# Performance work log

Measured on AMD Instinct MI355X. Metric: run time of the kernel, lower is better.

The kernel has to match this reference:

```python
import jax, jax.numpy as jnp
from jax import lax
import numpy as np

B, N, FIN, T, K, C_CHEB, F_TIME, STRIDE = 32, 900, 16, 24, 3, 64, 64, 1
LN_EPS = 1e-5


def _cheb_polys(L_tilde, K):
    # Faithful to repo: recurrence uses ELEMENTWISE multiply (np.ndarray '*').
    polys = [np.identity(N), np.asarray(L_tilde)]
    for i in range(2, K):
        polys.append(2 * L_tilde * polys[i - 1] - polys[i - 2])
    return np.stack(polys, axis=0).astype(np.float32)  # (K, N, N)


def setup_inputs() -> dict:
    key = jax.random.key(0)
    ks = jax.random.split(key, 6)
    rng = np.random.RandomState(0)
    A = rng.randn(N, N).astype(np.float32)
    L_tilde = (A + A.T) / (2.0 * np.sqrt(N))  # symmetric, entries O(1/sqrt(N))
    cheb = jnp.asarray(_cheb_polys(L_tilde, K))  # (K, N, N)
    x = jax.random.normal(ks[0], (B, N, FIN, T), dtype=jnp.float32)
    theta = jax.random.normal(ks[1], (K, FIN, C_CHEB), dtype=jnp.float32) * 0.1
    time_w = jax.random.normal(ks[2], (F_TIME, C_CHEB, 1, 3), dtype=jnp.float32) * 0.05
    time_b = jax.random.normal(ks[3], (F_TIME,), dtype=jnp.float32) * 0.01
    res_w = jax.random.normal(ks[4], (F_TIME, FIN, 1, 1), dtype=jnp.float32) * 0.1
    res_b = jax.random.normal(ks[5], (F_TIME,), dtype=jnp.float32) * 0.01
    gamma = jnp.ones((F_TIME,), dtype=jnp.float32)
    beta = jnp.zeros((F_TIME,), dtype=jnp.float32)
    return {"x": x, "cheb": cheb, "theta": theta, "time_w": time_w,
            "time_b": time_b, "res_w": res_w, "res_b": res_b,
            "gamma": gamma, "beta": beta}


def reference(x, cheb, theta, time_w, time_b, res_w, res_b, gamma, beta):
    b, n, f_in, t = x.shape
    # forward hardcodes spatial attention to ones
    spatial_at = jnp.ones((b, n, n), dtype=x.dtype)
    # Chebyshev graph conv with (trivial) spatial attention.
    # rhs[b,t,n,f] = sum_m (T_k * sA)[b,m,n] * x[b,m,f,t]
    out = jnp.zeros((b, t, n, theta.shape[-1]), dtype=x.dtype)
    for k in range(theta.shape[0]):
        Tk = cheb[k] * spatial_at                      # (B, N, N)
        rhs = jnp.einsum('bmn,bmft->btnf', Tk, x)      # (B, T, N, F_in)
        out = out + jnp.einsum('btnf,fc->btnc', rhs, theta[k])
    spatial_gcn = jax.nn.relu(out)                     # (B, T, N, C)
    # time conv over T axis: input layout (B, C, N, T), kernel (1,3), pad (0,1)
    g = jnp.transpose(spatial_gcn, (0, 3, 2, 1))       # (B, C, N, T)
    tc = lax.conv_general_dilated(g, time_w, window_strides=(1, STRIDE),
                                  padding=((0, 0), (1, 1)),
                                  dimension_numbers=('NCHW', 'OIHW', 'NCHW'))
    tc = tc + time_b[None, :, None, None]
    # residual 1x1 conv on raw input
    xr = jnp.transpose(x, (0, 2, 1, 3))                # (B, F_in, N, T)
    rc = lax.conv_general_dilated(xr, res_w, window_strides=(1, STRIDE),
                                  padding=((0, 0), (0, 0)),
                                  dimension_numbers=('NCHW', 'OIHW', 'NCHW'))
    rc = rc + res_b[None, :, None, None]
    y = jax.nn.relu(rc + tc)                           # (B, F_time, N, T)
    y = jnp.transpose(y, (0, 3, 2, 1))                 # (B, T, N, F_time)
    mu = jnp.mean(y, axis=-1, keepdims=True)
    var = jnp.mean(jnp.square(y - mu), axis=-1, keepdims=True)
    y_ln = (y - mu) * lax.rsqrt(var + LN_EPS) * gamma + beta
    return jnp.transpose(y_ln, (0, 2, 3, 1))           # (B, N, F_time, T)
```

## Files before the change

### kernel.cpp

```cpp
#include <hip/hip_runtime.h>
#include <hip/hip_bf16.h>

#define B_ 32
#define N_ 900
#define BN 8
#define NTILES 113
#define MS 16
#define MP 960

typedef __attribute__((ext_vector_type(8))) short bf16x8;
typedef __attribute__((ext_vector_type(16))) float f32x16;

#define OFF_XT 0u
#define OFF_CT 23592960u
#define OFF_XC 27279360u
#define OFF_TH 74465280u
#define OFF_TW 74472448u
#define WS_NEED 74500096u

__global__ __launch_bounds__(256)
void k0a_xT(const float* __restrict__ x, __hip_bfloat16* __restrict__ xT)
{
    __shared__ __hip_bfloat16 L[32][390];
    const int tid = threadIdx.x;
    const int m0 = blockIdx.x * 32, b = blockIdx.y;
#pragma unroll
    for (int it = 0; it < 12; ++it) {
        const int idx = tid + it * 256;
        const int mm = idx / 96, c4 = idx - mm * 96;
        float4 v = make_float4(0.f, 0.f, 0.f, 0.f);
        if (m0 + mm < N_)
            v = ((const float4*)(x + ((size_t)b * N_ + m0 + mm) * 384))[c4];
        L[mm][c4 * 4 + 0] = __float2bfloat16(v.x);
        L[mm][c4 * 4 + 1] = __float2bfloat16(v.y);
        L[mm][c4 * 4 + 2] = __float2bfloat16(v.z);
        L[mm][c4 * 4 + 3] = __float2bfloat16(v.w);
    }
    __syncthreads();
#pragma unroll
    for (int it = 0; it < 48; ++it) {
        const int idx = tid + it * 256;
        const int c = idx >> 5, mm = idx & 31;
        xT[((size_t)b * 384 + c) * MP + m0 + mm] = L[mm][c];
    }
}

__global__ __launch_bounds__(256)
void k0b_chebT(const float* __restrict__ cheb, __hip_bfloat16* __restrict__ chebT)
{
    __shared__ float L[32][33];
    const int tid = threadIdx.x;
    const int m0 = blockIdx.x * 32, n0 = blockIdx.y * 32, k = blockIdx.z;
#pragma unroll
    for (int it = 0; it < 4; ++it) {
        const int idx = tid + it * 256;
        const int mm = idx >> 5, nn = idx & 31;
        float v = 0.f;
        if (m0 + mm < N_ && n0 + nn < N_)
            v = cheb[(size_t)(k + 1) * (N_ * N_) + (size_t)(m0 + mm) * N_ + n0 + nn];
        L[mm][nn] = v;
    }
    __syncthreads();
#pragma unroll
    for (int it = 0; it < 4; ++it) {
        const int idx = tid + it * 256;
        const int nn = idx >> 5, mm = idx & 31;
        chebT[((size_t)k * MP + n0 + nn) * MP + m0 + mm] = __float2bfloat16(L[mm][nn]);
    }
}

__global__ __launch_bounds__(256)
void k0c_w(const float* __restrict__ tw, const float* __restrict__ rw,
           const float* __restrict__ th,
           __hip_bfloat16* __restrict__ thT, __hip_bfloat16* __restrict__ twB)
{
    const int tid = threadIdx.x;
    for (int i = tid; i < 64 * 56; i += 256) {
        const int c = i / 56, k = i - (i / 56) * 56;
        const float v = (k < 48) ? th[k * 64 + c] : 0.f;
        thT[i] = __float2bfloat16(v);
    }
    for (int i = tid; i < 64 * 216; i += 256) {
        const int co = i / 216, k = i - co * 216;
        float v = 0.f;
        if (k < 192)      v = tw[co * 192 + (k & 63) * 3 + (k >> 6)];
        else if (k < 208) v = rw[co * 16 + (k - 192)];
        twB[i] = __float2bfloat16(v);
    }
}

__global__ __launch_bounds__(512)
void k1_mfma(const __hip_bfloat16* __restrict__ xT,
             const __hip_bfloat16* __restrict__ chebT,
             __hip_bfloat16* __restrict__ xcb)
{
    __shared__ __align__(16) __hip_bfloat16 At[2][192][40];
    __shared__ __align__(16) __hip_bfloat16 Bt[2][128][40];
    const int tid = threadIdx.x;
    const int id  = blockIdx.x;
    const int swz  = (id & 7) * 120 + (id >> 3);
    const int tile = swz % 15;
    const int z    = swz / 15;
    const int n0 = (tile % 5) * 192;
    const int c0 = (tile / 5) * 128;
    const int b = z >> 1, k = z & 1;

    const int wid = tid >> 6, lane = tid & 63;
    const int wr = wid & 1, wc = wid >> 1;
    const int lr = lane & 31, hi = lane >> 5;

    const __hip_bfloat16* Asrc = chebT + ((size_t)k * MP + n0) * MP;
    const __hip_bfloat16* Bsrc = xT + ((size_t)b * 384 + c0) * MP;

    f32x16 acc[3];
#pragma unroll
    for (int rb = 0; rb < 3; ++rb)
#pragma unroll
        for (int j = 0; j < 16; ++j) acc[rb][j] = 0.f;

    auto stage = [&](int buf, int m0) {
        for (int q = tid; q < 768; q += 512) {
            const int r = q >> 2, c8 = (q & 3) * 8;
            *(int4*)&At[buf][r][c8] = *(const int4*)(Asrc + (size_t)r * MP + m0 + c8);
        }
        {
            const int q = tid;
            if (q < 512) {
                const int r = q >> 2, c8 = (q & 3) * 8;
                *(int4*)&Bt[buf][r][c8] = *(const int4*)(Bsrc + (size_t)r * MP + m0 + c8);
            }
        }
    };

    stage(0, 0);
    __syncthreads();
    for (int s = 0; s < 30; ++s) {
        if (s + 1 < 30) stage((s + 1) & 1, (s + 1) * 32);
        const int cur = s & 1;
#pragma unroll
        for (int ks = 0; ks < 2; ++ks) {
            const bf16x8 bb = *(const bf16x8*)&Bt[cur][wc * 32 + lr][ks * 16 + hi * 8];
#pragma unroll
            for (int rb = 0; rb < 3; ++rb) {
                const bf16x8 a =
                    *(const bf16x8*)&At[cur][wr * 96 + rb * 32 + lr][ks * 16 + hi * 8];
                acc[rb] = __builtin_amdgcn_mfma_f32_32x32x16_bf16(a, bb, acc[rb], 0, 0, 0);
            }
        }
        __syncthreads();
    }

    const int c = c0 + wc * 32 + lr;
    __hip_bfloat16* ob = xcb + ((size_t)(k * B_ + b)) * (MP * 384) + c;
#pragma unroll
    for (int rb = 0; rb < 3; ++rb)
#pragma unroll
        for (int reg = 0; reg < 16; ++reg) {
            const int row = n0 + wr * 96 + rb * 32 + (reg & 3) + 8 * (reg >> 2) + 4 * hi;
            ob[(size_t)row * 384] = __float2bfloat16(acc[rb][reg]);
        }
}

__global__ __launch_bounds__(384, 5)
void k2_mfma(const float* __restrict__ x,
             const __hip_bfloat16* __restrict__ xcb,
             const __hip_bfloat16* __restrict__ thT,
             const __hip_bfloat16* __restrict__ twB,
             const float* __restrict__ tb, const float* __restrict__ rb,
             const float* __restrict__ gam, const float* __restrict__ bet,
             float* __restrict__ out)
{
    __shared__ __align__(16) short xcL[2][8][384];
    __shared__ __align__(16) __hip_bfloat16 xbL[8][24][24];
    __shared__ __align__(16) __hip_bfloat16 gcnL[8][26][72];
    __shared__ float biasL[64], gamL[64], betL[64];

    const int tid = threadIdx.x;
    const int wid = tid >> 6, lane = tid & 63;
    const int l31 = lane & 31, hi = lane >> 5;
    const int n_base = blockIdx.x * BN;
    const int b = blockIdx.y;

    if (tid < 64) {
        biasL[tid] = tb[tid] + rb[tid];
        gamL[tid]  = gam[tid];
        betL[tid]  = bet[tid];
    }
    for (int q = tid; q < 768; q += 384) {
        const int kk = q / 384, r = q - kk * 384;
        const int nl = r / 48, ch = r - nl * 48;
        ((int4*)xcL)[q] =
            *(const int4*)(xcb + (((size_t)(kk * B_ + b)) * MP + n_base + nl) * 384 + ch * 8);
    }
    for (int i = tid; i < 768; i += 384) {
        const int nl = i / 96, rem = i - nl * 96, f = rem / 6, t4 = rem - f * 6;
        const int ng = n_base + nl;
        float4 v = make_float4(0.f, 0.f, 0.f, 0.f);
        if (ng < N_)
            v = ((const float4*)(x + ((size_t)b * N_ + ng) * 384 + f * 24))[t4];
        xbL[nl][t4 * 4 + 0][f] = __float2bfloat16(v.x);
        xbL[nl][t4 * 4 + 1][f] = __float2bfloat16(v.y);
        xbL[nl][t4 * 4 + 2][f] = __float2bfloat16(v.z);
        xbL[nl][t4 * 4 + 3][f] = __float2bfloat16(v.w);
    }
    for (int i = tid; i < 1024; i += 384) {
        const int nl = i >> 7, c = (i >> 1) & 63, e = i & 1;
        gcnL[nl][e ? 25 : 0][c] = __float2bfloat16(0.f);
    }

    const int colA = wid * 32 + l31;
    const int nlA = colA / 24, tA = colA - nlA * 24;

    __syncthreads();

    const bf16x8 b0 = *(const bf16x8*)&xbL[nlA][tA][hi * 8];
    bf16x8 b1, b2;
#pragma unroll
    for (int j = 0; j < 8; ++j) {
        b1[j] = xcL[0][nlA][(hi * 8 + j) * 24 + tA];
        b2[j] = xcL[1][nlA][(hi * 8 + j) * 24 + tA];
    }

    {
        const short* thg = (const short*)thT;
        f32x16 a0, a1;
#pragma unroll
        for (int j = 0; j < 16; ++j) { a0[j] = 0.f; a1[j] = 0.f; }
        bf16x8 af;
        af = *(const bf16x8*)(thg + l31 * 56 + hi * 8);
        a0 = __builtin_amdgcn_mfma_f32_32x32x16_bf16(af, b0, a0, 0, 0, 0);
        af = *(const bf16x8*)(thg + l31 * 56 + 16 + hi * 8);
        a0 = __builtin_amdgcn_mfma_f32_32x32x16_bf16(af, b1, a0, 0, 0, 0);
        af = *(const bf16x8*)(thg + l31 * 56 + 32 + hi * 8);
        a0 = __builtin_amdgcn_mfma_f32_32x32x16_bf16(af, b2, a0, 0, 0, 0);
        af = *(const bf16x8*)(thg + (32 + l31) * 56 + hi * 8);
        a1 = __builtin_amdgcn_mfma_f32_32x32x16_bf16(af, b0, a1, 0, 0, 0);
        af = *(const bf16x8*)(thg + (32 + l31) * 56 + 16 + hi * 8);
        a1 = __builtin_amdgcn_mfma_f32_32x32x16_bf16(af, b1, a1, 0, 0, 0);
        af = *(const bf16x8*)(thg + (32 + l31) * 56 + 32 + hi * 8);
        a1 = __builtin_amdgcn_mfma_f32_32x32x16_bf16(af, b2, a1, 0, 0, 0);
#pragma unroll
        for (int reg = 0; reg < 16; ++reg) {
            const int cr = (reg & 3) + 8 * (reg >> 2) + 4 * hi;
            gcnL[nlA][tA + 1][cr]      = __float2bfloat16(fmaxf(a0[reg], 0.f));
            gcnL[nlA][tA + 1][32 + cr] = __float2bfloat16(fmaxf(a1[reg], 0.f));
        }
    }
    __syncthreads();

    const short* twg = (const short*)twB;
    f32x16 acc0, acc1;
#pragma unroll
    for (int j = 0; j < 16; ++j) { acc0[j] = 0.f; acc1[j] = 0.f; }
#pragma unroll
    for (int s = 0; s < 12; ++s) {
        const int dt  = s >> 2;
        const int ci0 = (s & 3) * 16 + hi * 8;
        const bf16x8 bb = *(const bf16x8*)&gcnL[nlA][tA + dt][ci0];
        const bf16x8 a0 = *(const bf16x8*)(twg + l31 * 216 + dt * 64 + ci0);
        const bf16x8 a1 = *(const bf16x8*)(twg + (32 + l31) * 216 + dt * 64 + ci0);
        acc0 = __builtin_amdgcn_mfma_f32_32x32x16_bf16(a0, bb, acc0, 0, 0, 0);
        acc1 = __builtin_amdgcn_mfma_f32_32x32x16_bf16(a1, bb, acc1, 0, 0, 0);
    }
    {
        const bf16x8 a0 = *(const bf16x8*)(twg + l31 * 216 + 192 + hi * 8);
        const bf16x8 a1 = *(const bf16x8*)(twg + (32 + l31) * 216 + 192 + hi * 8);
        acc0 = __builtin_amdgcn_mfma_f32_32x32x16_bf16(a0, b0, acc0, 0, 0, 0);
        acc1 = __builtin_amdgcn_mfma_f32_32x32x16_bf16(a1, b0, acc1, 0, 0, 0);
    }

    float y0[16], y1[16];
    float s1 = 0.f, s2 = 0.f;
#pragma unroll
    for (int reg = 0; reg < 16; ++reg) {
        const int cr = (reg & 3) + 8 * (reg >> 2) + 4 * hi;
        const float v0 = fmaxf(acc0[reg] + biasL[cr], 0.f);
        const float v1 = fmaxf(acc1[reg] + biasL[32 + cr], 0.f);
        y0[reg] = v0; y1[reg] = v1;
        s1 += v0 + v1;
        s2 += v0 * v0 + v1 * v1;
    }
    s1 += __shfl_xor(s1, 32);
    s2 += __shfl_xor(s2, 32);
    const float mu  = s1 * (1.f / 64.f);
    const float var = fmaxf(s2 * (1.f / 64.f) - mu * mu, 0.f);
    const float rs  = rsqrtf(var + 1e-5f);

    const int ng = n_base + nlA;
    if (ng < N_) {
        float* op = out + ((size_t)b * N_ + ng) * 1536 + tA;
#pragma unroll
        for (int reg = 0; reg < 16; ++reg) {
            const int cr = (reg & 3) + 8 * (reg >> 2) + 4 * hi;
            op[(size_t)cr * 24]        = (y0[reg] - mu) * rs * gamL[cr] + betL[cr];
            op[(size_t)(32 + cr) * 24] = (y1[reg] - mu) * rs * gamL[32 + cr] + betL[32 + cr];
        }
    }
}

__global__ __launch_bounds__(256, 2)
void astgcn_fused(const float* __restrict__ x, const float* __restrict__ cheb,
                  const float* __restrict__ theta, const float* __restrict__ tw,
                  const float* __restrict__ tb, const float* __restrict__ rw,
                  const float* __restrict__ rb, const float* __restrict__ gam,
                  const float* __restrict__ bet, float* __restrict__ out)
{
    __shared__ __align__(16) unsigned char smem[57152];
    float* xc   = (float*)smem;
    unsigned char* Y = smem + 24576;
    float* rwl  = (float*)(smem + 52032);
    float* misc = (float*)(smem + 56128);

    const int tid = threadIdx.x;
    const int n_base = blockIdx.x * BN;
    const int b = blockIdx.y;

    if (tid < 64) {
        misc[tid]       = tb[tid];
        misc[64 + tid]  = rb[tid];
        misc[128 + tid] = gam[tid];
        misc[192 + tid] = bet[tid];
    }
    for (int i = tid; i < 1024; i += 256) {
        const int co = i & 63, f = i >> 6;
        rwl[f * 64 + co] = rw[co * 16 + f];
    }

    float* xs  = (float*)Y;
    float* wls = (float*)(Y + 24576);
    const int nloc = tid >> 5;
    const int cg   = tid & 31;
    float a1[12], a2[12];
#pragma unroll
    for (int j = 0; j < 12; ++j) { a1[j] = 0.f; a2[j] = 0.f; }
    const float* xb = x + (size_t)b * N_ * 384;

    for (int mc = 0; mc < N_; mc += MS) {
        const int mlim = (N_ - mc) < MS ? (N_ - mc) : MS;
        __syncthreads();
        for (int i = tid; i < mlim * 96; i += 256) {
            const int mm = i / 96, c4 = i - mm * 96;
            ((float4*)(xs + mm * 384))[c4] =
                ((const float4*)(xb + (size_t)(mc + mm) * 384))[c4];
        }
        for (int i = tid; i < 2 * MS * 8; i += 256) {
            const int k = i >> 7, mm = (i >> 3) & 15, nn = i & 7;
            const int ng = n_base + nn;
            float wv = 0.f;
            if (mm < mlim && ng < N_)
                wv = cheb[(size_t)(k + 1) * (N_ * N_) + (size_t)(mc + mm) * N_ + ng];
            wls[(k * MS + mm) * 8 + nn] = wv;
        }
        __syncthreads();
        for (int mm = 0; mm < mlim; ++mm) {
            const float w1 = wls[mm * 8 + nloc];
            const float w2 = wls[(MS + mm) * 8 + nloc];
            const float* xr = xs + mm * 384 + (cg << 2);
#pragma unroll
            for (int seg = 0; seg < 3; ++seg) {
                const float4 v = *(const float4*)(xr + seg * 128);
                a1[seg*4+0] = fmaf(w1, v.x, a1[seg*4+0]);
                a1[seg*4+1] = fmaf(w1, v.y, a1[seg*4+1]);
                a1[seg*4+2] = fmaf(w1, v.z, a1[seg*4+2]);
                a1[seg*4+3] = fmaf(w1, v.w, a1[seg*4+3]);
                a2[seg*4+0] = fmaf(w2, v.x, a2[seg*4+0]);
                a2[seg*4+1] = fmaf(w2, v.y, a2[seg*4+1]);
                a2[seg*4+2] = fmaf(w2, v.z, a2[seg*4+2]);
                a2[seg*4+3] = fmaf(w2, v.w, a2[seg*4+3]);
            }
        }
    }
    __syncthreads();
#pragma unroll
    for (int seg = 0; seg < 3; ++seg) {
#pragma unroll
        for (int jj = 0; jj < 4; ++jj) {
            const int c = seg * 128 + (cg << 2) + jj;
            const int f = c / 24, t = c - f * 24;
            xc[(nloc * 24 + t) * 16 + f]        = a1[seg * 4 + jj];
            xc[((BN + nloc) * 24 + t) * 16 + f] = a2[seg * 4 + jj];
        }
    }
    __syncthreads();

    __hip_bfloat16* gcn = (__hip_bfloat16*)Y;
    {
        const int c2 = tid & 63;
        const int pg = tid >> 6;
        float th0r[16], th1r[16], th2r[16];
#pragma unroll
        for (int f = 0; f < 16; ++f) {
            th0r[f] = theta[f * 64 + c2];
            th1r[f] = theta[(16 + f) * 64 + c2];
            th2r[f] = theta[(32 + f) * 64 + c2];
        }
        for (int i = 0; i < 48; ++i) {
            const int p  = pg + 4 * i;
            const int nl = p / 24, t = p - nl * 24;
            const int ng = n_base + nl;
            float o = 0.f;
            if (ng < N_) {
                const float* xg = x + ((size_t)b * N_ + ng) * 384 + t;
                const float* x1 = xc + (nl * 24 + t) * 16;
                const float* x2 = xc + ((BN + nl) * 24 + t) * 16;
#pragma unroll
                for (int f = 0; f < 16; ++f)
                    o = fmaf(xg[f * 24], th0r[f], o);
#pragma unroll
                for (int f = 0; f < 16; ++f)
                    o = fmaf(x1[f], th1r[f], fmaf(x2[f], th2r[f], o));
            }
            o = fmaxf(o, 0.f);
            gcn[(nl * 26 + t + 1) * 66 + c2] = __float2bfloat16(o);
            if (t == 0)  gcn[(nl * 26) * 66 + c2]      = __float2bfloat16(0.f);
            if (t == 23) gcn[(nl * 26 + 25) * 66 + c2] = __float2bfloat16(0.f);
        }
    }

    const int nl3 = tid / 24, t3 = tid - nl3 * 24;
    const int ng3 = n_base + nl3;
    const bool act = (tid < 192) && (ng3 < N_);
    float acc[64];
#pragma unroll
    for (int co = 0; co < 64; ++co) acc[co] = misc[co] + misc[64 + co];
    if (act) {
        const float* xg = x + ((size_t)b * N_ + ng3) * 384 + t3;
#pragma unroll
        for (int f = 0; f < 16; ++f) {
            const float xv = xg[f * 24];
            const float* rp = rwl + f * 64;
#pragma unroll
            for (int co = 0; co < 64; ++co) acc[co] = fmaf(xv, rp[co], acc[co]);
        }
    }
    float* twl = xc;
#pragma unroll
    for (int half = 0; half < 2; ++half) {
        __syncthreads();
        for (int i = tid; i < 6144; i += 256)
            twl[i] = tw[((half * 32) + (i & 31)) * 192 + ((i >> 5) & 63) * 3 + (i >> 11)];
        __syncthreads();
        if (act) {
            const __hip_bfloat16* g0 = gcn + (nl3 * 26 + t3) * 66;
#pragma unroll
            for (int dt = 0; dt < 3; ++dt) {
                const __hip_bfloat16* grow = g0 + dt * 66;
                for (int ci = 0; ci < 64; ++ci) {
                    const float g = __bfloat162float(grow[ci]);
                    const float* twp = twl + (dt * 64 + ci) * 32;
#pragma unroll
                    for (int j = 0; j < 32; ++j)
                        acc[half * 32 + j] = fmaf(g, twp[j], acc[half * 32 + j]);
                }
            }
        }
    }
    if (act) {
        float mu = 0.f;
#pragma unroll
        for (int co = 0; co < 64; ++co) { acc[co] = fmaxf(acc[co], 0.f); mu += acc[co]; }
        mu *= (1.f / 64.f);
        float var = 0.f;
#pragma unroll
        for (int co = 0; co < 64; ++co) { const float d = acc[co] - mu; var = fmaf(d, d, var); }
        var *= (1.f / 64.f);
        const float rs = rsqrtf(var + 1e-5f);
        float* op = out + ((size_t)b * N_ + ng3) * (64 * 24) + t3;
#pragma unroll
        for (int co = 0; co < 64; ++co) {
            const float yl = (acc[co] - mu) * rs * misc[128 + co] + misc[192 + co];
            op[(size_t)co * 24] = yl;
        }
    }
}

extern "C" void kernel_launch(void* const* d_in, const int* in_sizes, int n_in,
                              void* d_out, int out_size, void* d_ws, size_t ws_size,
                              hipStream_t stream) {
    (void)out_size;
    const float *px = nullptr, *pcheb = nullptr, *pth = nullptr,
                *ptw = nullptr, *prw = nullptr;
    const float* p64[4] = {nullptr, nullptr, nullptr, nullptr};
    int n64 = 0;
    for (int i = 0; i < n_in; ++i) {
        const float* p = (const float*)d_in[i];
        switch (in_sizes[i]) {
            case 11059200: px    = p; break;
            case 2430000:  pcheb = p; break;
            case 3072:     pth   = p; break;
            case 12288:    ptw   = p; break;
            case 1024:     prw   = p; break;
            case 64:       if (n64 < 4) p64[n64] = p; ++n64; break;
            default: break;
        }
    }
    if (!px || !pcheb || !pth || !ptw || !prw || n64 != 4) {
        px    = (const float*)d_in[0]; pcheb = (const float*)d_in[1];
        pth   = (const float*)d_in[2]; ptw   = (const float*)d_in[3];
        p64[0] = (const float*)d_in[4]; prw  = (const float*)d_in[5];
        p64[1] = (const float*)d_in[6]; p64[2] = (const float*)d_in[7];
        p64[3] = (const float*)d_in[8];
    }
    float* out = (float*)d_out;

    if (ws_size >= (size_t)WS_NEED) {
        unsigned char* ws = (unsigned char*)d_ws;
        __hip_bfloat16* xT    = (__hip_bfloat16*)(ws + OFF_XT);
        __hip_bfloat16* chebT = (__hip_bfloat16*)(ws + OFF_CT);
        __hip_bfloat16* xcb   = (__hip_bfloat16*)(ws + OFF_XC);
        __hip_bfloat16* thT   = (__hip_bfloat16*)(ws + OFF_TH);
        __hip_bfloat16* twB   = (__hip_bfloat16*)(ws + OFF_TW);

        k0a_xT   <<<dim3(30, B_),     256, 0, stream>>>(px, xT);
        k0b_chebT<<<dim3(30, 30, 2),  256, 0, stream>>>(pcheb, chebT);
        k0c_w    <<<1,                256, 0, stream>>>(ptw, prw, pth, thT, twB);
        k1_mfma  <<<960,              512, 0, stream>>>(xT, chebT, xcb);
        k2_mfma  <<<dim3(NTILES, B_), 384, 0, stream>>>(px, xcb, thT, twB,
                                                        p64[0], p64[1], p64[2], p64[3], out);
    } else {
        astgcn_fused<<<dim3(NTILES, B_), 256, 0, stream>>>(px, pcheb, pth, ptw,
                                                           p64[0], prw, p64[1],
                                                           p64[2], p64[3], out);
    }
}
```

Measured before the change: 198.6 us.

## Process four node tiles per k2 block with register prefetch of next tile

The final fused kernel now loops over four consecutive node tiles per block instead of one, shrinking the grid from 113 to 29 blocks along the node axis. While the current tile runs its graph-conv and time-conv MFMAs, the next tile's xcb and x data are loaded into registers and then written to shared memory after the current tile's reads finish. The aim is to hide global-load latency and amortise block setup such as the bias, gamma and beta loads and the pad zeroing. The trade-off is fewer resident blocks for latency hiding, an extra barrier per tile, more register pressure, and three surplus padded tiles at the end that are masked on output.

```diff
diff --git a/kernel.cpp b/kernel.cpp
--- a/kernel.cpp
+++ b/kernel.cpp
@@ -178,123 +178,151 @@
     const int tid = threadIdx.x;
     const int wid = tid >> 6, lane = tid & 63;
     const int l31 = lane & 31, hi = lane >> 5;
-    const int n_base = blockIdx.x * BN;
     const int b = blockIdx.y;
+    const int tile0 = blockIdx.x * 4;
 
     if (tid < 64) {
         biasL[tid] = tb[tid] + rb[tid];
         gamL[tid]  = gam[tid];
         betL[tid]  = bet[tid];
     }
-    for (int q = tid; q < 768; q += 384) {
-        const int kk = q / 384, r = q - kk * 384;
-        const int nl = r / 48, ch = r - nl * 48;
-        ((int4*)xcL)[q] =
-            *(const int4*)(xcb + (((size_t)(kk * B_ + b)) * MP + n_base + nl) * 384 + ch * 8);
-    }
-    for (int i = tid; i < 768; i += 384) {
-        const int nl = i / 96, rem = i - nl * 96, f = rem / 6, t4 = rem - f * 6;
-        const int ng = n_base + nl;
-        float4 v = make_float4(0.f, 0.f, 0.f, 0.f);
-        if (ng < N_)
-            v = ((const float4*)(x + ((size_t)b * N_ + ng) * 384 + f * 24))[t4];
-        xbL[nl][t4 * 4 + 0][f] = __float2bfloat16(v.x);
-        xbL[nl][t4 * 4 + 1][f] = __float2bfloat16(v.y);
-        xbL[nl][t4 * 4 + 2][f] = __float2bfloat16(v.z);
-        xbL[nl][t4 * 4 + 3][f] = __float2bfloat16(v.w);
-    }
     for (int i = tid; i < 1024; i += 384) {
         const int nl = i >> 7, c = (i >> 1) & 63, e = i & 1;
         gcnL[nl][e ? 25 : 0][c] = __float2bfloat16(0.f);
     }
 
+    int4   rxc[2];
+    float4 rx[2];
+    auto ldregs = [&](int tile) {
+        const int nb = tile * BN;
+#pragma unroll
+        for (int u = 0; u < 2; ++u) {
+            const int q = tid + u * 384;
+            const int kk = q / 384, r = q - kk * 384;
+            const int nl = r / 48, ch = r - nl * 48;
+            rxc[u] = *(const int4*)(xcb + (((size_t)(kk * B_ + b)) * MP + nb + nl) * 384 + ch * 8);
+        }
+#pragma unroll
+        for (int u = 0; u < 2; ++u) {
+            const int i = tid + u * 384;
+            const int nl = i / 96, rem = i - nl * 96, f = rem / 6, t4 = rem - f * 6;
+            const int ng = nb + nl;
+            rx[u] = (ng < N_)
+                ? ((const float4*)(x + ((size_t)b * N_ + ng) * 384 + f * 24))[t4]
+                : make_float4(0.f, 0.f, 0.f, 0.f);
+        }
+    };
+    auto dswrite = [&]() {
+#pragma unroll
+        for (int u = 0; u < 2; ++u) ((int4*)xcL)[tid + u * 384] = rxc[u];
+#pragma unroll
+        for (int u = 0; u < 2; ++u) {
+            const int i = tid + u * 384;
+            const int nl = i / 96, rem = i - nl * 96, f = rem / 6, t4 = rem - f * 6;
+            xbL[nl][t4 * 4 + 0][f] = __float2bfloat16(rx[u].x);
+            xbL[nl][t4 * 4 + 1][f] = __float2bfloat16(rx[u].y);
+            xbL[nl][t4 * 4 + 2][f] = __float2bfloat16(rx[u].z);
+            xbL[nl][t4 * 4 + 3][f] = __float2bfloat16(rx[u].w);
+        }
+    };
+
     const int colA = wid * 32 + l31;
     const int nlA = colA / 24, tA = colA - nlA * 24;
 
+    ldregs(tile0);
+    dswrite();
     __syncthreads();
 
-    const bf16x8 b0 = *(const bf16x8*)&xbL[nlA][tA][hi * 8];
-    bf16x8 b1, b2;
-#pragma unroll
-    for (int j = 0; j < 8; ++j) {
-        b1[j] = xcL[0][nlA][(hi * 8 + j) * 24 + tA];
-        b2[j] = xcL[1][nlA][(hi * 8 + j) * 24 + tA];
-    }
-
-    {
-        const short* thg = (const short*)thT;
-        f32x16 a0, a1;
-#pragma unroll
-        for (int j = 0; j < 16; ++j) { a0[j] = 0.f; a1[j] = 0.f; }
-        bf16x8 af;
-        af = *(const bf16x8*)(thg + l31 * 56 + hi * 8);
-        a0 = __builtin_amdgcn_mfma_f32_32x32x16_bf16(af, b0, a0, 0, 0, 0);
-        af = *(const bf16x8*)(thg + l31 * 56 + 16 + hi * 8);
-        a0 = __builtin_amdgcn_mfma_f32_32x32x16_bf16(af, b1, a0, 0, 0, 0);
-        af = *(const bf16x8*)(thg + l31 * 56 + 32 + hi * 8);
-        a0 = __builtin_amdgcn_mfma_f32_32x32x16_bf16(af, b2, a0, 0, 0, 0);
-        af = *(const bf16x8*)(thg + (32 + l31) * 56 + hi * 8);
-        a1 = __builtin_amdgcn_mfma_f32_32x32x16_bf16(af, b0, a1, 0, 0, 0);
-        af = *(const bf16x8*)(thg + (32 + l31) * 56 + 16 + hi * 8);
-        a1 = __builtin_amdgcn_mfma_f32_32x32x16_bf16(af, b1, a1, 0, 0, 0);
-        af = *(const bf16x8*)(thg + (32 + l31) * 56 + 32 + hi * 8);
-        a1 = __builtin_amdgcn_mfma_f32_32x32x16_bf16(af, b2, a1, 0, 0, 0);
+    for (int j = 0; j < 4; ++j) {
+        const int tile = tile0 + j;
+
+        const bf16x8 b0 = *(const bf16x8*)&xbL[nlA][tA][hi * 8];
+        bf16x8 b1, b2;
+#pragma unroll
+        for (int jj = 0; jj < 8; ++jj) {
+            b1[jj] = xcL[0][nlA][(hi * 8 + jj) * 24 + tA];
+            b2[jj] = xcL[1][nlA][(hi * 8 + jj) * 24 + tA];
+        }
+        if (j < 3) ldregs(tile + 1);
+
+        {
+            const short* thg = (const short*)thT;
+            f32x16 a0, a1;
+#pragma unroll
+            for (int jj = 0; jj < 16; ++jj) { a0[jj] = 0.f; a1[jj] = 0.f; }
+            bf16x8 af;
+            af = *(const bf16x8*)(thg + l31 * 56 + hi * 8);
+            a0 = __builtin_amdgcn_mfma_f32_32x32x16_bf16(af, b0, a0, 0, 0, 0);
+            af = *(const bf16x8*)(thg + l31 * 56 + 16 + hi * 8);
+            a0 = __builtin_amdgcn_mfma_f32_32x32x16_bf16(af, b1, a0, 0, 0, 0);
+            af = *(const bf16x8*)(thg + l31 * 56 + 32 + hi * 8);
+            a0 = __builtin_amdgcn_mfma_f32_32x32x16_bf16(af, b2, a0, 0, 0, 0);
+            af = *(const bf16x8*)(thg + (32 + l31) * 56 + hi * 8);
+            a1 = __builtin_amdgcn_mfma_f32_32x32x16_bf16(af, b0, a1, 0, 0, 0);
+            af = *(const bf16x8*)(thg + (32 + l31) * 56 + 16 + hi * 8);
+            a1 = __builtin_amdgcn_mfma_f32_32x32x16_bf16(af, b1, a1, 0, 0, 0);
+            af = *(const bf16x8*)(thg + (32 + l31) * 56 + 32 + hi * 8);
+            a1 = __builtin_amdgcn_mfma_f32_32x32x16_bf16(af, b2, a1, 0, 0, 0);
+#pragma unroll
+            for (int reg = 0; reg < 16; ++reg) {
+                const int cr = (reg & 3) + 8 * (reg >> 2) + 4 * hi;
+                gcnL[nlA][tA + 1][cr]      = __float2bfloat16(fmaxf(a0[reg], 0.f));
+                gcnL[nlA][tA + 1][32 + cr] = __float2bfloat16(fmaxf(a1[reg], 0.f));
+            }
+        }
+        __syncthreads();
+
+        const short* twg = (const short*)twB;
+        f32x16 acc0, acc1;
+#pragma unroll
+        for (int jj = 0; jj < 16; ++jj) { acc0[jj] = 0.f; acc1[jj] = 0.f; }
+#pragma unroll
+        for (int s = 0; s < 12; ++s) {
+            const int dt  = s >> 2;
+            const int ci0 = (s & 3) * 16 + hi * 8;
+            const bf16x8 bb = *(const bf16x8*)&gcnL[nlA][tA + dt][ci0];
+            const bf16x8 a0 = *(const bf16x8*)(twg + l31 * 216 + dt * 64 + ci0);
+            const bf16x8 a1 = *(const bf16x8*)(twg + (32 + l31) * 216 + dt * 64 + ci0);
+            acc0 = __builtin_amdgcn_mfma_f32_32x32x16_bf16(a0, bb, acc0, 0, 0, 0);
+            acc1 = __builtin_amdgcn_mfma_f32_32x32x16_bf16(a1, bb, acc1, 0, 0, 0);
+        }
+        {
+            const bf16x8 a0 = *(const bf16x8*)(twg + l31 * 216 + 192 + hi * 8);
+            const bf16x8 a1 = *(const bf16x8*)(twg + (32 + l31) * 216 + 192 + hi * 8);
+            acc0 = __builtin_amdgcn_mfma_f32_32x32x16_bf16(a0, b0, acc0, 0, 0, 0);
+            acc1 = __builtin_amdgcn_mfma_f32_32x32x16_bf16(a1, b0, acc1, 0, 0, 0);
+        }
+
+        if (j < 3) dswrite();
+
+        float y0[16], y1[16];
+        float s1 = 0.f, s2 = 0.f;
 #pragma unroll
         for (int reg = 0; reg < 16; ++reg) {
             const int cr = (reg & 3) + 8 * (reg >> 2) + 4 * hi;
-            gcnL[nlA][tA + 1][cr]      = __float2bfloat16(fmaxf(a0[reg], 0.f));
-            gcnL[nlA][tA + 1][32 + cr] = __float2bfloat16(fmaxf(a1[reg], 0.f));
-        }
-    }
-    __syncthreads();
-
-    const short* twg = (const short*)twB;
-    f32x16 acc0, acc1;
-#pragma unroll
-    for (int j = 0; j < 16; ++j) { acc0[j] = 0.f; acc1[j] = 0.f; }
-#pragma unroll
-    for (int s = 0; s < 12; ++s) {
-        const int dt  = s >> 2;
-        const int ci0 = (s & 3) * 16 + hi * 8;
-        const bf16x8 bb = *(const bf16x8*)&gcnL[nlA][tA + dt][ci0];
-        const bf16x8 a0 = *(const bf16x8*)(twg + l31 * 216 + dt * 64 + ci0);
-        const bf16x8 a1 = *(const bf16x8*)(twg + (32 + l31) * 216 + dt * 64 + ci0);
-        acc0 = __builtin_amdgcn_mfma_f32_32x32x16_bf16(a0, bb, acc0, 0, 0, 0);
-        acc1 = __builtin_amdgcn_mfma_f32_32x32x16_bf16(a1, bb, acc1, 0, 0, 0);
-    }
-    {
-        const bf16x8 a0 = *(const bf16x8*)(twg + l31 * 216 + 192 + hi * 8);
-        const bf16x8 a1 = *(const bf16x8*)(twg + (32 + l31) * 216 + 192 + hi * 8);
-        acc0 = __builtin_amdgcn_mfma_f32_32x32x16_bf16(a0, b0, acc0, 0, 0, 0);
-        acc1 = __builtin_amdgcn_mfma_f32_32x32x16_bf16(a1, b0, acc1, 0, 0, 0);
-    }
-
-    float y0[16], y1[16];
-    float s1 = 0.f, s2 = 0.f;
-#pragma unroll
-    for (int reg = 0; reg < 16; ++reg) {
-        const int cr = (reg & 3) + 8 * (reg >> 2) + 4 * hi;
-        const float v0 = fmaxf(acc0[reg] + biasL[cr], 0.f);
-        const float v1 = fmaxf(acc1[reg] + biasL[32 + cr], 0.f);
-        y0[reg] = v0; y1[reg] = v1;
-        s1 += v0 + v1;
-        s2 += v0 * v0 + v1 * v1;
-    }
-    s1 += __shfl_xor(s1, 32);
-    s2 += __shfl_xor(s2, 32);
-    const float mu  = s1 * (1.f / 64.f);
-    const float var = fmaxf(s2 * (1.f / 64.f) - mu * mu, 0.f);
-    const float rs  = rsqrtf(var + 1e-5f);
-
-    const int ng = n_base + nlA;
-    if (ng < N_) {
-        float* op = out + ((size_t)b * N_ + ng) * 1536 + tA;
-#pragma unroll
-        for (int reg = 0; reg < 16; ++reg) {
-            const int cr = (reg & 3) + 8 * (reg >> 2) + 4 * hi;
-            op[(size_t)cr * 24]        = (y0[reg] - mu) * rs * gamL[cr] + betL[cr];
-            op[(size_t)(32 + cr) * 24] = (y1[reg] - mu) * rs * gamL[32 + cr] + betL[32 + cr];
-        }
+            const float v0 = fmaxf(acc0[reg] + biasL[cr], 0.f);
+            const float v1 = fmaxf(acc1[reg] + biasL[32 + cr], 0.f);
+            y0[reg] = v0; y1[reg] = v1;
+            s1 += v0 + v1;
+            s2 += v0 * v0 + v1 * v1;
+        }
+        s1 += __shfl_xor(s1, 32);
+        s2 += __shfl_xor(s2, 32);
+        const float mu  = s1 * (1.f / 64.f);
+        const float var = fmaxf(s2 * (1.f / 64.f) - mu * mu, 0.f);
+        const float rs  = rsqrtf(var + 1e-5f);
+
+        const int ng = tile * BN + nlA;
+        if (ng < N_) {
+            float* op = out + ((size_t)b * N_ + ng) * 1536 + tA;
+#pragma unroll
+            for (int reg = 0; reg < 16; ++reg) {
+                const int cr = (reg & 3) + 8 * (reg >> 2) + 4 * hi;
+                op[(size_t)cr * 24]        = (y0[reg] - mu) * rs * gamL[cr] + betL[cr];
+                op[(size_t)(32 + cr) * 24] = (y1[reg] - mu) * rs * gamL[32 + cr] + betL[32 + cr];
+            }
+        }
+        __syncthreads();
     }
 }
 
@@ -515,7 +543,7 @@
         k0b_chebT<<<dim3(30, 30, 2),  256, 0, stream>>>(pcheb, chebT);
         k0c_w    <<<1,                256, 0, stream>>>(ptw, prw, pth, thT, twB);
         k1_mfma  <<<960,              512, 0, stream>>>(xT, chebT, xcb);
-        k2_mfma  <<<dim3(NTILES, B_), 384, 0, stream>>>(px, xcb, thT, twB,
+        k2_mfma  <<<dim3(29, B_),     384, 0, stream>>>(px, xcb, thT, twB,
                                                         p64[0], p64[1], p64[2], p64[3], out);
     } else {
         astgcn_fused<<<dim3(NTILES, B_), 256, 0, stream>>>(px, pcheb, pth, ptw,
```

New measurement: 470.1 us. 137% more time.
